# Kernel optimization log

Measured on AMD Instinct MI355X. Metric: run time of the kernel, lower is better.

Reference implementation:

```python
import jax, jax.numpy as jnp
import numpy as np

JUMP = 0.05      # stride 'jumps'
FILTER = 0.15    # filter_dim per axis
PTS = 20         # arange(0, 1, 0.05) -> 20 positions per dim -> 400 centers


def _centers():
    g = jnp.arange(PTS, dtype=jnp.float32) * JUMP  # start=0, domain=1, direction=+1
    xx, yy = jnp.meshgrid(g, g, indexing="ij")
    return jnp.stack([xx.ravel(), yy.ravel()], axis=-1)  # [400, 2]


def setup_inputs() -> dict:
    key = jax.random.key(0)
    ks = jax.random.split(key, 10)
    B, H, N = 64, 256, 2048
    F = 2    # input_numb_field * output_numb_field = 2*1 kernel nets
    KH = 20  # default kernel hidden width

    def w(k, shape, fan_in):
        return jax.random.normal(k, shape, jnp.float32) / np.sqrt(fan_in)

    return dict(
        weights=jax.random.normal(ks[0], (B, H), jnp.float32),
        grid=jax.random.uniform(ks[1], (N, 2), jnp.float32),
        # FeedForward: H -> 120 -> 240 -> 400, Tanh activations
        ff_w1=w(ks[2], (H, 120), H), ff_b1=jnp.zeros((120,), jnp.float32),
        ff_w2=w(ks[3], (120, 240), 120), ff_b2=jnp.zeros((240,), jnp.float32),
        ff_w3=w(ks[4], (240, 400), 240), ff_b3=jnp.zeros((400,), jnp.float32),
        # per-field kernel MLPs: 2 -> 20 -> 20 -> 1 (ReLU), stacked on F
        k_w1=w(ks[5], (F, 2, KH), 2), k_b1=jnp.zeros((F, KH), jnp.float32),
        k_w2=w(ks[6], (F, KH, KH), KH), k_b2=jnp.zeros((F, KH), jnp.float32),
        k_w3=w(ks[7], (F, KH, 1), KH), k_b3=jnp.zeros((F, 1), jnp.float32),
    )


def reference(weights, grid, ff_w1, ff_b1, ff_w2, ff_b2, ff_w3, ff_b3,
              k_w1, k_b1, k_w2, k_b2, k_w3, k_b3):
    # 1) FeedForward: latent weights -> 400 per-stride integrals
    h = jnp.tanh(weights @ ff_w1 + ff_b1)
    h = jnp.tanh(h @ ff_w2 + ff_b2)
    integ = h @ ff_w3 + ff_b3                       # [B, 400]

    # 2) continuous transpose convolution onto the point cloud `grid`
    centers = _centers()                            # [K=400, 2]
    local = grid[:, None, :] - centers[None, :, :]  # [N, K, 2] filter-local coords
    inside = jnp.all((local >= 0.0) & (local <= FILTER), axis=-1)  # [N, K]

    # kernel MLPs evaluated densely over (point, center) pairs, masked to window
    t = jax.nn.relu(jnp.einsum('nkd,fdh->fnkh', local, k_w1) + k_b1[:, None, None, :])
    t = jax.nn.relu(jnp.einsum('fnkh,fhg->fnkg', t, k_w2) + k_b2[:, None, None, :])
    kval = jnp.einsum('fnkg,fg->fnk', t, k_w3[:, :, 0]) + k_b3[:, :, None]  # [F, N, K]
    kval = jnp.where(inside[None], kval, 0.0)

    # spread integrals through the (masked) continuous filters
    fields = jnp.einsum('fnk,bk->bnf', kval, integ)  # [B, N, F]
    return jax.nn.sigmoid(fields)
```

## Files before the change

### kernel.cpp

```cpp
#include <hip/hip_runtime.h>
#include <math.h>

#define NPTS 2048
#define KDIM 400

__global__ __launch_bounds__(512) void k_ff_and_kval(
    const float* __restrict__ weights, const float* __restrict__ grid,
    const float* __restrict__ ff_w1, const float* __restrict__ ff_b1,
    const float* __restrict__ ff_w2, const float* __restrict__ ff_b2,
    const float* __restrict__ ff_w3, const float* __restrict__ ff_b3,
    const float* __restrict__ k_w1, const float* __restrict__ k_b1,
    const float* __restrict__ k_w2, const float* __restrict__ k_b2,
    const float* __restrict__ k_w3, const float* __restrict__ k_b3,
    float* __restrict__ integ, float* __restrict__ kv0,
    float* __restrict__ kv1, int* __restrict__ kidx)
{
    const int t = threadIdx.x;
    if (blockIdx.x < 128) {
        const int b    = blockIdx.x >> 1;
        const int half = blockIdx.x & 1;
        __shared__ float wrow[256];
        __shared__ float h1[120];
        __shared__ float h2[240];
        __shared__ float p1[4][120];
        __shared__ float p2[2][240];
        __shared__ float p3[2][200];

        if (t < 256) wrow[t] = weights[b * 256 + t];
        __syncthreads();

        if (t < 480) {
            const int seg = t / 120;
            const int o   = t - seg * 120;
            float s = (seg == 0) ? ff_b1[o] : 0.f;
            const int i0 = seg * 64;
            #pragma unroll 16
            for (int i = 0; i < 64; ++i)
                s = fmaf(wrow[i0 + i], ff_w1[(i0 + i) * 120 + o], s);
            p1[seg][o] = s;
        }
        __syncthreads();
        if (t < 120) h1[t] = tanhf(p1[0][t] + p1[1][t] + p1[2][t] + p1[3][t]);
        __syncthreads();

        if (t < 480) {
            const int seg = t / 240;
            const int o   = t - seg * 240;
            float s = (seg == 0) ? ff_b2[o] : 0.f;
            const int i0 = seg * 60;
            #pragma unroll 15
            for (int i = 0; i < 60; ++i)
                s = fmaf(h1[i0 + i], ff_w2[(i0 + i) * 240 + o], s);
            p2[seg][o] = s;
        }
        __syncthreads();
        if (t < 240) h2[t] = tanhf(p2[0][t] + p2[1][t]);
        __syncthreads();

        if (t < 400) {
            const int seg = t / 200;
            const int o   = t - seg * 200;
            const int oc  = half * 200 + o;
            float s = (seg == 0) ? ff_b3[oc] : 0.f;
            const int i0 = seg * 120;
            #pragma unroll 15
            for (int i = 0; i < 120; ++i)
                s = fmaf(h2[i0 + i], ff_w3[(i0 + i) * 400 + oc], s);
            p3[seg][o] = s;
        }
        __syncthreads();
        if (t < 200) integ[b * 400 + half * 200 + t] = p3[0][t] + p3[1][t];
    } else {
        __shared__ float sw1[80], sb1[40], sw2[800], sb2[40], sw3[40], sb3[2];
        for (int i = t; i < 80;  i += 512) sw1[i] = k_w1[i];
        for (int i = t; i < 800; i += 512) sw2[i] = k_w2[i];
        if (t < 40) { sb1[t] = k_b1[t]; sb2[t] = k_b2[t]; sw3[t] = k_w3[t]; }
        if (t < 2)  sb3[t] = k_b3[t];
        __syncthreads();

        const int pid  = blockIdx.x - 128;
        const int n    = pid * 32 + (t & 31);
        const int slot = t >> 5;
        const float2 g2 = ((const float2*)grid)[n];
        const float x = g2.x, y = g2.y;
        const int ilx = (int)ceilf((x - 0.15f) * 20.0f - 0.01f);
        const int ily = (int)ceilf((y - 0.15f) * 20.0f - 0.01f);
        const int ix = ilx + (slot >> 2);
        const int iy = ily + (slot & 3);

        float kva = 0.f, kvb = 0.f;
        int k = 0;
        if (ix >= 0 && ix < 20 && iy >= 0 && iy < 20) {
            const float gx = __fmul_rn((float)ix, 0.05f);
            const float gy = __fmul_rn((float)iy, 0.05f);
            const float lx = __fsub_rn(x, gx);
            const float ly = __fsub_rn(y, gy);
            if (lx >= 0.f && lx <= 0.15f && ly >= 0.f && ly <= 0.15f) {
                k = ix * 20 + iy;
                #pragma unroll
                for (int f = 0; f < 2; ++f) {
                    float hv[20];
                    #pragma unroll
                    for (int hh = 0; hh < 20; ++hh)
                        hv[hh] = fmaxf(0.f,
                            fmaf(lx, sw1[f * 40 + hh],
                            fmaf(ly, sw1[f * 40 + 20 + hh], sb1[f * 20 + hh])));
                    float o = sb3[f];
                    #pragma unroll
                    for (int g = 0; g < 20; ++g) {
                        float s = sb2[f * 20 + g];
                        #pragma unroll
                        for (int hh = 0; hh < 20; ++hh)
                            s = fmaf(hv[hh], sw2[f * 400 + hh * 20 + g], s);
                        o = fmaf(fmaxf(0.f, s), sw3[f * 20 + g], o);
                    }
                    if (f == 0) kva = o; else kvb = o;
                }
            }
        }
        kv0 [slot * NPTS + n] = kva;
        kv1 [slot * NPTS + n] = kvb;
        kidx[slot * NPTS + n] = k;
    }
}

__global__ __launch_bounds__(256) void k_field(
    const float* __restrict__ integ, const float* __restrict__ kv0,
    const float* __restrict__ kv1, const int* __restrict__ kidx,
    float2* __restrict__ out)
{
    const int tid = blockIdx.x * 256 + threadIdx.x;
    const int b = tid >> 11;
    const int n = tid & (NPTS - 1);
    const float* __restrict__ irow = integ + b * KDIM;
    float a0 = 0.f, a1 = 0.f;
    #pragma unroll
    for (int j = 0; j < 16; ++j) {
        const int k = kidx[j * NPTS + n];
        const float w = irow[k];
        a0 = fmaf(kv0[j * NPTS + n], w, a0);
        a1 = fmaf(kv1[j * NPTS + n], w, a1);
    }
    out[tid] = make_float2(1.f / (1.f + __expf(-a0)),
                           1.f / (1.f + __expf(-a1)));
}

extern "C" void kernel_launch(void* const* d_in, const int* in_sizes, int n_in,
                              void* d_out, int out_size, void* d_ws, size_t ws_size,
                              hipStream_t stream) {
    const float* weights = (const float*)d_in[0];
    const float* grid    = (const float*)d_in[1];
    const float* ff_w1   = (const float*)d_in[2];
    const float* ff_b1   = (const float*)d_in[3];
    const float* ff_w2   = (const float*)d_in[4];
    const float* ff_b2   = (const float*)d_in[5];
    const float* ff_w3   = (const float*)d_in[6];
    const float* ff_b3   = (const float*)d_in[7];
    const float* k_w1    = (const float*)d_in[8];
    const float* k_b1    = (const float*)d_in[9];
    const float* k_w2    = (const float*)d_in[10];
    const float* k_b2    = (const float*)d_in[11];
    const float* k_w3    = (const float*)d_in[12];
    const float* k_b3    = (const float*)d_in[13];

    float* integ = (float*)d_ws;
    float* kv0   = integ + 64 * KDIM;
    float* kv1   = kv0 + 16 * NPTS;
    int*   kidx  = (int*)(kv1 + 16 * NPTS);

    k_ff_and_kval<<<128 + 64, 512, 0, stream>>>(
        weights, grid, ff_w1, ff_b1, ff_w2, ff_b2, ff_w3, ff_b3,
        k_w1, k_b1, k_w2, k_b2, k_w3, k_b3,
        integ, kv0, kv1, kidx);

    k_field<<<(64 * NPTS) / 256, 256, 0, stream>>>(
        integ, kv0, kv1, kidx, (float2*)d_out);
}
```

Baseline: 15.71 us.

## Split kernel-MLP work per field across threads and stage integrals in LDS

The kernel-value section now assigns each of the two field MLPs to a separate half of the block. Each block covers 16 points instead of 32 and the launch grows to 256 blocks, which halves the serial per-thread MLP chain and adds blocks to spread across CUs. The field kernel now uses 512-thread blocks, one batch row per four blocks, and stages that row's 400 integrals in shared memory so the indexed gathers read LDS rather than global memory. The cost is recomputing the grid and window indices per field, plus an extra sync and shared-memory fill in the second kernel.

```diff
diff --git a/kernel.cpp b/kernel.cpp
--- a/kernel.cpp
+++ b/kernel.cpp
@@ -17,21 +17,15 @@
 {
     const int t = threadIdx.x;
     if (blockIdx.x < 128) {
-        const int b    = blockIdx.x >> 1;
-        const int half = blockIdx.x & 1;
-        __shared__ float wrow[256];
-        __shared__ float h1[120];
-        __shared__ float h2[240];
-        __shared__ float p1[4][120];
-        __shared__ float p2[2][240];
-        __shared__ float p3[2][200];
+        const int b = blockIdx.x >> 1, half = blockIdx.x & 1;
+        __shared__ float wrow[256], h1[120], h2[240];
+        __shared__ float p1[4][120], p2[2][240], p3[2][200];
 
         if (t < 256) wrow[t] = weights[b * 256 + t];
         __syncthreads();
 
         if (t < 480) {
-            const int seg = t / 120;
-            const int o   = t - seg * 120;
+            const int seg = t / 120, o = t - seg * 120;
             float s = (seg == 0) ? ff_b1[o] : 0.f;
             const int i0 = seg * 64;
             #pragma unroll 16
@@ -44,8 +38,7 @@
         __syncthreads();
 
         if (t < 480) {
-            const int seg = t / 240;
-            const int o   = t - seg * 240;
+            const int seg = t / 240, o = t - seg * 240;
             float s = (seg == 0) ? ff_b2[o] : 0.f;
             const int i0 = seg * 60;
             #pragma unroll 15
@@ -58,9 +51,7 @@
         __syncthreads();
 
         if (t < 400) {
-            const int seg = t / 200;
-            const int o   = t - seg * 200;
-            const int oc  = half * 200 + o;
+            const int seg = t / 200, o = t - seg * 200, oc = half * 200 + o;
             float s = (seg == 0) ? ff_b3[oc] : 0.f;
             const int i0 = seg * 120;
             #pragma unroll 15
@@ -79,8 +70,11 @@
         __syncthreads();
 
         const int pid  = blockIdx.x - 128;
-        const int n    = pid * 32 + (t & 31);
-        const int slot = t >> 5;
+        const int f    = t >> 8;
+        const int idx  = t & 255;
+        const int slot = idx >> 4;
+        const int pt   = idx & 15;
+        const int n    = pid * 16 + pt;
         const float2 g2 = ((const float2*)grid)[n];
         const float x = g2.x, y = g2.y;
         const int ilx = (int)ceilf((x - 0.15f) * 20.0f - 0.01f);
@@ -88,7 +82,7 @@
         const int ix = ilx + (slot >> 2);
         const int iy = ily + (slot & 3);
 
-        float kva = 0.f, kvb = 0.f;
+        float kv = 0.f;
         int k = 0;
         if (ix >= 0 && ix < 20 && iy >= 0 && iy < 20) {
             const float gx = __fmul_rn((float)ix, 0.05f);
@@ -97,52 +91,49 @@
             const float ly = __fsub_rn(y, gy);
             if (lx >= 0.f && lx <= 0.15f && ly >= 0.f && ly <= 0.15f) {
                 k = ix * 20 + iy;
+                float hv[20];
                 #pragma unroll
-                for (int f = 0; f < 2; ++f) {
-                    float hv[20];
+                for (int hh = 0; hh < 20; ++hh)
+                    hv[hh] = fmaxf(0.f,
+                        fmaf(lx, sw1[f * 40 + hh],
+                        fmaf(ly, sw1[f * 40 + 20 + hh], sb1[f * 20 + hh])));
+                float o = sb3[f];
+                #pragma unroll
+                for (int g = 0; g < 20; ++g) {
+                    float s = sb2[f * 20 + g];
                     #pragma unroll
                     for (int hh = 0; hh < 20; ++hh)
-                        hv[hh] = fmaxf(0.f,
-                            fmaf(lx, sw1[f * 40 + hh],
-                            fmaf(ly, sw1[f * 40 + 20 + hh], sb1[f * 20 + hh])));
-                    float o = sb3[f];
-                    #pragma unroll
-                    for (int g = 0; g < 20; ++g) {
-                        float s = sb2[f * 20 + g];
-                        #pragma unroll
-                        for (int hh = 0; hh < 20; ++hh)
-                            s = fmaf(hv[hh], sw2[f * 400 + hh * 20 + g], s);
-                        o = fmaf(fmaxf(0.f, s), sw3[f * 20 + g], o);
-                    }
-                    if (f == 0) kva = o; else kvb = o;
+                        s = fmaf(hv[hh], sw2[f * 400 + hh * 20 + g], s);
+                    o = fmaf(fmaxf(0.f, s), sw3[f * 20 + g], o);
                 }
+                kv = o;
             }
         }
-        kv0 [slot * NPTS + n] = kva;
-        kv1 [slot * NPTS + n] = kvb;
-        kidx[slot * NPTS + n] = k;
+        (f ? kv1 : kv0)[slot * NPTS + n] = kv;
+        if (f == 0) kidx[slot * NPTS + n] = k;
     }
 }
 
-__global__ __launch_bounds__(256) void k_field(
+__global__ __launch_bounds__(512) void k_field(
     const float* __restrict__ integ, const float* __restrict__ kv0,
     const float* __restrict__ kv1, const int* __restrict__ kidx,
     float2* __restrict__ out)
 {
-    const int tid = blockIdx.x * 256 + threadIdx.x;
-    const int b = tid >> 11;
-    const int n = tid & (NPTS - 1);
-    const float* __restrict__ irow = integ + b * KDIM;
+    __shared__ float Li[KDIM];
+    const int b  = blockIdx.x >> 2;
+    const int n  = (blockIdx.x & 3) * 512 + threadIdx.x;
+    if (threadIdx.x < KDIM) Li[threadIdx.x] = integ[b * KDIM + threadIdx.x];
+    __syncthreads();
+
     float a0 = 0.f, a1 = 0.f;
     #pragma unroll
     for (int j = 0; j < 16; ++j) {
-        const int k = kidx[j * NPTS + n];
-        const float w = irow[k];
+        const float w = Li[kidx[j * NPTS + n]];
         a0 = fmaf(kv0[j * NPTS + n], w, a0);
         a1 = fmaf(kv1[j * NPTS + n], w, a1);
     }
-    out[tid] = make_float2(1.f / (1.f + __expf(-a0)),
-                           1.f / (1.f + __expf(-a1)));
+    out[b * NPTS + n] = make_float2(1.f / (1.f + __expf(-a0)),
+                                    1.f / (1.f + __expf(-a1)));
 }
 
 extern "C" void kernel_launch(void* const* d_in, const int* in_sizes, int n_in,
@@ -168,11 +159,11 @@
     float* kv1   = kv0 + 16 * NPTS;
     int*   kidx  = (int*)(kv1 + 16 * NPTS);
 
-    k_ff_and_kval<<<128 + 64, 512, 0, stream>>>(
+    k_ff_and_kval<<<256, 512, 0, stream>>>(
         weights, grid, ff_w1, ff_b1, ff_w2, ff_b2, ff_w3, ff_b3,
         k_w1, k_b1, k_w2, k_b2, k_w3, k_b3,
         integ, kv0, kv1, kidx);
 
-    k_field<<<(64 * NPTS) / 256, 256, 0, stream>>>(
+    k_field<<<256, 512, 0, stream>>>(
         integ, kv0, kv1, kidx, (float2*)d_out);
 }
```

After: 15.09 us. -3.9%, faster.
